# Performance work log

Hardware: AMD Instinct MI355X
Metric: run time of the kernel (lower is better)

Reference implementation:

```python
import jax, jax.numpy as jnp
import numpy as np

B, S, H, D = 2, 4096, 16, 128
TILE = 128
T = S // TILE          # 32 tiles
TOPK = 7               # anchor-selected tiles per query tile (local tile appended -> 8)
DM = H * D
NEG = -1e10


def setup_inputs() -> dict:
    key = jax.random.key(0)
    ks = jax.random.split(key, 6)
    x = jax.random.normal(ks[0], (B, S, DM), dtype=jnp.float32)
    wq = jax.random.normal(ks[1], (DM, H * D), dtype=jnp.float32) * 0.02
    wk = jax.random.normal(ks[2], (DM, H * D), dtype=jnp.float32) * 0.02
    wv = jax.random.normal(ks[3], (DM, H * D), dtype=jnp.float32) * 0.02
    wo = jax.random.normal(ks[4], (H * D, DM), dtype=jnp.float32) * 0.02
    # RoPE tables (real/imag of freqs_cis), LLaMA-style
    inv_freq = 1.0 / (10000.0 ** (np.arange(0, D, 2, dtype=np.float32) / D))  # [D/2]
    t = np.arange(S, dtype=np.float32)
    freqs = np.outer(t, inv_freq)  # [S, D/2]
    cos = jnp.asarray(np.cos(freqs), dtype=jnp.float32)
    sin = jnp.asarray(np.sin(freqs), dtype=jnp.float32)
    anchor_indices = jax.random.randint(ks[5], (B, H, T, TOPK), 0, T, dtype=jnp.int32)
    return {"x": x, "wq": wq, "wk": wk, "wv": wv, "wo": wo,
            "cos": cos, "sin": sin, "anchor_indices": anchor_indices}


def _apply_rope(q, k, cos, sin):
    # q,k: [B,H,S,D]; cos,sin: [S,D/2]
    cos_f = jnp.concatenate([cos, cos], axis=-1)[None, None]  # [1,1,S,D]
    sin_f = jnp.concatenate([sin, sin], axis=-1)[None, None]

    def rot_half(x):
        h = x.shape[-1] // 2
        return jnp.concatenate([-x[..., h:], x[..., :h]], axis=-1)

    return q * cos_f + rot_half(q) * sin_f, k * cos_f + rot_half(k) * sin_f


def reference(x, wq, wk, wv, wo, cos, sin, anchor_indices):
    b, s, _ = x.shape
    h = anchor_indices.shape[1]
    t = anchor_indices.shape[2]
    tile = s // t
    d = wq.shape[1] // h

    q = (x @ wq).reshape(b, s, h, d).transpose(0, 2, 1, 3)  # [B,H,S,D]
    k = (x @ wk).reshape(b, s, h, d).transpose(0, 2, 1, 3)
    v = (x @ wv).reshape(b, s, h, d).transpose(0, 2, 1, 3)
    q, k = _apply_rope(q, k, cos, sin)

    # append local tile to anchor-selected tiles -> [B,H,T,K+1]
    local = jnp.broadcast_to(jnp.arange(t, dtype=jnp.int32)[None, None, :, None], (b, h, t, 1))
    tile_sel = jnp.concatenate([anchor_indices, local], axis=-1)
    # token indices of gathered tiles: [B,H,T,(K+1)*tile]
    offs = jnp.arange(tile, dtype=jnp.int32)[None, None, None, None, :]
    tok_idx = (tile_sel[..., None] * tile + offs)
    sparse_len = tile_sel.shape[-1] * tile
    flat_idx = jnp.clip(tok_idx.reshape(b, h, t, sparse_len), 0, s - 1)

    # gather K/V tiles: [B,H,T,L,D]
    gid = flat_idx.reshape(b, h, t * sparse_len)
    k_sp = jnp.take_along_axis(k, gid[..., None], axis=2).reshape(b, h, t, sparse_len, d)
    v_sp = jnp.take_along_axis(v, gid[..., None], axis=2).reshape(b, h, t, sparse_len, d)

    q_t = q.reshape(b, h, t, tile, d)
    logits = jnp.einsum('bhtqd,bhtkd->bhtqk', q_t, k_sp) / jnp.sqrt(jnp.float32(d))

    # causal future-mask within gathered set
    q_pos = jnp.arange(s, dtype=jnp.int32).reshape(t, tile)
    fut = flat_idx[:, :, :, None, :] > q_pos[None, None, :, :, None]  # [B,H,T,tile,L]
    logits = jnp.where(fut, NEG, logits)
    weights = jax.nn.softmax(logits, axis=-1)
    all_masked = jnp.all(fut, axis=-1, keepdims=True)
    weights = jnp.where(all_masked, 0.0, weights)
    weights = jnp.where(jnp.isnan(weights), 0.0, weights)

    out = jnp.einsum('bhtqk,bhtkd->bhtqd', weights, v_sp)
    out = out.reshape(b, h, s, d).transpose(0, 2, 1, 3).reshape(b, s, h * d)
    return out @ wo
```

## Files before the change

### kernel.cpp

```cpp
#include <hip/hip_runtime.h>
#include <hip/hip_bf16.h>


typedef __bf16 bf16_t;
using bf16x8 = __attribute__((ext_vector_type(8))) __bf16;
using bf16x4 = __attribute__((ext_vector_type(4))) __bf16;
using f32x4  = __attribute__((ext_vector_type(4))) float;

typedef const __attribute__((address_space(1))) void* gas_ptr;
typedef __attribute__((address_space(3))) void* las_ptr;

__device__ __forceinline__ void async_copy16(const void* g, void* l) {
  __builtin_amdgcn_global_load_lds((gas_ptr)g, (las_ptr)l, 16, 0, 0);
}

__device__ __forceinline__ f32x4 mfma16x16x32(bf16x8 a, bf16x8 b, f32x4 c) {
  return __builtin_amdgcn_mfma_f32_16x16x32_bf16(a, b, c, 0, 0, 0);
}

__global__ void prep_kernel(const float* __restrict__ x, const float* __restrict__ wq,
                            const float* __restrict__ wk, const float* __restrict__ wv,
                            const float* __restrict__ wo, bf16_t* __restrict__ xb,
                            bf16_t* __restrict__ wcat, bf16_t* __restrict__ wot) {
  __shared__ bf16_t t[64][66];
  const int bidx = blockIdx.x;
  if (bidx >= 4096) {
    int idx = (bidx - 4096) * 256 + threadIdx.x;
    float4 v = ((const float4*)x)[idx];
    bf16x4 r;
    r.x = (bf16_t)v.x; r.y = (bf16_t)v.y; r.z = (bf16_t)v.z; r.w = (bf16_t)v.w;
    ((bf16x4*)xb)[idx] = r;
    return;
  }
  const int z = bidx >> 10, bt = bidx & 1023;
  const float* W = (z == 0) ? wq : (z == 1) ? wk : (z == 2) ? wv : wo;
  bf16_t* Wt = (z == 3) ? wot : (wcat + (size_t)z * 2048 * 2048);
  const int r0 = (bt >> 5) * 64, c0 = (bt & 31) * 64;
  const int tx = threadIdx.x & 63, ty = threadIdx.x >> 6;
  #pragma unroll
  for (int i = 0; i < 16; ++i) {
    int r = ty + 4 * i;
    t[r][tx] = (bf16_t)W[(size_t)(r0 + r) * 2048 + c0 + tx];
  }
  __syncthreads();
  #pragma unroll
  for (int i = 0; i < 16; ++i) {
    int n = ty + 4 * i;
    Wt[(size_t)(c0 + n) * 2048 + r0 + tx] = t[tx][n];
  }
}

__global__ __launch_bounds__(512, 2) void gemm256(
    const bf16_t* __restrict__ A, const bf16_t* __restrict__ Bt,
    int nb, int mode, float* __restrict__ Cf,
    bf16_t* __restrict__ outQ, bf16_t* __restrict__ outK,
    bf16_t* __restrict__ outVT,
    const float* __restrict__ cosT, const float* __restrict__ sinT)
{
  __shared__ bf16_t Apan[2][16384];
  __shared__ bf16_t Bpan[2][16384];
  const int bid = blockIdx.x;
  const int cpx = gridDim.x >> 3;
  const int swz = (bid & 7) * cpx + (bid >> 3);
  const int RM = cpx / nb;
  const int bm = ((swz / cpx) * RM + (swz % RM)) * 256;
  const int bn = ((swz % cpx) / RM) * 256;
  const int tid = threadIdx.x;
  const int w = tid >> 6, l = tid & 63;
  const int wr = w >> 1, wc = w & 1;
  const int fr = l & 15, g4 = l >> 4;

  const bf16_t* aS[4];
  const bf16_t* bS[4];
  int dst[4];
  #pragma unroll
  for (int i = 0; i < 4; ++i) {
    int c = tid + i * 512;
    int row = c >> 3, ch = c & 7;
    int sc = (ch ^ (row & 7)) * 8;
    aS[i] = A  + (size_t)(bm + row) * 2048 + sc;
    bS[i] = Bt + (size_t)(bn + row) * 2048 + sc;
    dst[i] = c * 16;
  }

  int aOff[2][4], bOff[2][8];
  #pragma unroll
  for (int kc = 0; kc < 2; ++kc) {
    #pragma unroll
    for (int m = 0; m < 4; ++m) {
      int R = wr * 64 + m * 16 + fr;
      aOff[kc][m] = R * 128 + (((kc * 4 + g4) ^ (R & 7)) << 4);
    }
    #pragma unroll
    for (int n = 0; n < 8; ++n) {
      int R = wc * 128 + n * 16 + fr;
      bOff[kc][n] = R * 128 + (((kc * 4 + g4) ^ (R & 7)) << 4);
    }
  }

  f32x4 acc[4][8];
  #pragma unroll
  for (int m = 0; m < 4; ++m)
    #pragma unroll
    for (int n = 0; n < 8; ++n) acc[m][n] = (f32x4){0.f, 0.f, 0.f, 0.f};

  auto STAGE = [&](int t) {
    const int slot = t & 1;
    const int kb = t * 64;
    char* dA = (char*)&Apan[slot][0];
    char* dB = (char*)&Bpan[slot][0];
    #pragma unroll
    for (int i = 0; i < 4; ++i) {
      async_copy16(aS[i] + kb, dA + dst[i]);
      async_copy16(bS[i] + kb, dB + dst[i]);
    }
  };

  STAGE(0);
  __syncthreads();

  #pragma unroll 1
  for (int phi = 0; phi < 32; ++phi) {
    const int slot = phi & 1;
    const char* pa = (const char*)&Apan[slot][0];
    const char* pb = (const char*)&Bpan[slot][0];

    bf16x8 af0[4], bf0[8];
    #pragma unroll
    for (int m = 0; m < 4; ++m) af0[m] = *(const bf16x8*)(pa + aOff[0][m]);
    #pragma unroll
    for (int n = 0; n < 8; ++n) bf0[n] = *(const bf16x8*)(pb + bOff[0][n]);
    if (phi < 31) STAGE(phi + 1);
    __builtin_amdgcn_s_setprio(1);
    #pragma unroll
    for (int m = 0; m < 4; ++m)
      #pragma unroll
      for (int n = 0; n < 8; ++n)
        acc[m][n] = mfma16x16x32(af0[m], bf0[n], acc[m][n]);
    __builtin_amdgcn_s_setprio(0);

    bf16x8 af1[4], bf1[8];
    #pragma unroll
    for (int m = 0; m < 4; ++m) af1[m] = *(const bf16x8*)(pa + aOff[1][m]);
    #pragma unroll
    for (int n = 0; n < 8; ++n) bf1[n] = *(const bf16x8*)(pb + bOff[1][n]);
    __builtin_amdgcn_s_setprio(1);
    #pragma unroll
    for (int m = 0; m < 4; ++m)
      #pragma unroll
      for (int n = 0; n < 8; ++n)
        acc[m][n] = mfma16x16x32(af1[m], bf1[n], acc[m][n]);
    __builtin_amdgcn_s_setprio(0);

    asm volatile("s_waitcnt vmcnt(0)" ::: "memory");
    __builtin_amdgcn_sched_barrier(0);
    __builtin_amdgcn_s_barrier();
    __builtin_amdgcn_sched_barrier(0);
  }

  if (mode == 0) {
    float* S = (w < 4) ? (float*)((char*)&Apan[0][0] + w * 16384)
                       : (float*)((char*)&Bpan[0][0] + (w - 4) * 16384);
    #pragma unroll
    for (int h = 0; h < 2; ++h) {
      #pragma unroll
      for (int mm = 0; mm < 2; ++mm) {
        int m = h * 2 + mm;
        #pragma unroll
        for (int n = 0; n < 8; ++n)
          #pragma unroll
          for (int j = 0; j < 4; ++j)
            S[(mm * 16 + g4 * 4 + j) * 128 + n * 16 + fr] = acc[m][n][j];
      }
      #pragma unroll
      for (int r2 = 0; r2 < 32; ++r2) {
        float2 v = *(const float2*)&S[r2 * 128 + l * 2];
        int row = bm + wr * 64 + h * 32 + r2;
        *(float2*)&Cf[(size_t)row * 2048 + bn + wc * 128 + l * 2] = v;
      }
    }
    return;
  }

  const int colbase = bn + wc * 128;
  const int proj = colbase >> 11;
  const int hh = (colbase & 2047) >> 7;
  if (proj == 2) {
    #pragma unroll
    for (int m = 0; m < 4; ++m) {
      int row0 = bm + wr * 64 + m * 16 + g4 * 4;
      int b_ = row0 >> 12, sr = row0 & 4095;
      #pragma unroll
      for (int n = 0; n < 8; ++n) {
        int d_ = n * 16 + fr;
        bf16x4 pkv;
        #pragma unroll
        for (int j = 0; j < 4; ++j) pkv[j] = (bf16_t)acc[m][n][j];
        *(bf16x4*)&outVT[(((size_t)(b_ * 16 + hh)) * 128 + d_) * 4096 + sr] = pkv;
      }
    }
  } else {
    bf16_t* dst_ = proj ? outK : outQ;
    #pragma unroll
    for (int m = 0; m < 4; ++m) {
      int row0 = bm + wr * 64 + m * 16 + g4 * 4;
      int b_ = row0 >> 12, s0 = row0 & 4095;
      size_t hbase = ((size_t)(b_ * 16 + hh)) * 4096;
      #pragma unroll
      for (int n = 0; n < 4; ++n) {
        int d = n * 16 + fr;
        #pragma unroll
        for (int j = 0; j < 4; ++j) {
          int s = s0 + j;
          float c  = cosT[s * 64 + d];
          float sn = sinT[s * 64 + d];
          float x0 = acc[m][n][j], x1 = acc[m][n + 4][j];
          dst_[(hbase + s) * 128 + d]      = (bf16_t)(x0 * c - x1 * sn);
          dst_[(hbase + s) * 128 + d + 64] = (bf16_t)(x1 * c + x0 * sn);
        }
      }
    }
  }
}

__global__ __launch_bounds__(512, 4) void attn_kernel(
    const bf16_t* __restrict__ Qf, const bf16_t* __restrict__ Kf,
    const bf16_t* __restrict__ Vt, const int* __restrict__ anchors,
    bf16_t* __restrict__ outB)
{
  __shared__ bf16_t Kl[2][8192];
  __shared__ bf16_t Vl[2][8192];
  __shared__ bf16_t Pbuf[8][1024];
  const int orig = blockIdx.x;
  const int blk = (orig & 7) * 128 + (orig >> 3);
  const int qt = 31 - (blk & 31);
  const int h = (blk >> 5) & 15, b = blk >> 9;
  const int bh = b * 16 + h;
  const int tid = threadIdx.x, w = tid >> 6, l = tid & 63;
  const int fr = l & 15, g4 = l >> 4;
  const float scale = 0.08838834764831845f;

  const int* anc = anchors + ((size_t)bh * 32 + qt) * 7;
  unsigned long long pk = 0;
  int nt = 0;
  #pragma unroll
  for (int t = 0; t < 7; ++t) {
    int v = anc[t];
    if (v <= qt) { pk |= (unsigned long long)v << (5 * nt); ++nt; }
  }
  pk |= (unsigned long long)qt << (5 * nt); ++nt;
  const int NS = nt * 2;

  const bf16_t* Qbase = Qf + (size_t)bh * 4096 * 128;
  const bf16_t* Kbase = Kf + (size_t)bh * 4096 * 128;
  const bf16_t* Vbase = Vt + (size_t)bh * 128 * 4096;
  char* P = (char*)&Pbuf[w][0];

  auto STAGE = [&](int tb2, int p) {
    const bf16_t* ksrc = Kbase + (size_t)tb2 * 128;
    const bf16_t* vsrc = Vbase + tb2;
    char* kd = (char*)&Kl[p][0];
    char* vd = (char*)&Vl[p][0];
    #pragma unroll
    for (int i = 0; i < 2; ++i) {
      int c = tid + i * 512;
      int kr = c >> 4, kcol = c & 15;
      async_copy16(ksrc + (size_t)kr * 128 + (size_t)((kcol ^ (kr & 7)) * 8),
                   kd + c * 16);
      int vr = c >> 3, vcol = c & 7;
      async_copy16(vsrc + (size_t)vr * 4096 + (size_t)((vcol ^ (vr & 7)) * 8),
                   vd + c * 16);
    }
  };

  const int qrow = qt * 128 + w * 16 + fr;
  bf16x8 aq[4];
  #pragma unroll
  for (int kc = 0; kc < 4; ++kc)
    aq[kc] = *(const bf16x8*)(Qbase + (size_t)qrow * 128 + kc * 32 + g4 * 8);

  STAGE((int)(pk & 31) * 128, 0);
  __syncthreads();

  float mrun = -1e30f, lrun = 0.f;
  f32x4 o[8];
  #pragma unroll
  for (int nd = 0; nd < 8; ++nd) o[nd] = (f32x4){0.f, 0.f, 0.f, 0.f};

  for (int s = 0; s < NS; ++s) {
    const int p = s & 1;
    const int ts = (int)((pk >> (5 * (s >> 1))) & 31);
    const bool domask = (ts == qt);
    if (s + 1 < NS) {
      int s1 = s + 1;
      int ts1 = (int)((pk >> (5 * (s1 >> 1))) & 31);
      STAGE(ts1 * 128 + (s1 & 1) * 64, p ^ 1);
    }

    f32x4 sc[4];
    #pragma unroll
    for (int n = 0; n < 4; ++n) sc[n] = (f32x4){0.f, 0.f, 0.f, 0.f};
    #pragma unroll
    for (int kc = 0; kc < 4; ++kc) {
      bf16x8 kf[4];
      #pragma unroll
      for (int n = 0; n < 4; ++n) {
        int r = n * 16 + fr;
        kf[n] = *(const bf16x8*)((const char*)&Kl[p][0] +
                 r * 256 + (((kc * 4 + g4) ^ (r & 7)) << 4));
      }
      #pragma unroll
      for (int n = 0; n < 4; ++n)
        sc[n] = mfma16x16x32(kf[n], aq[kc], sc[n]);
    }

    float rmax = -1e30f;
    if (domask) {
      const int qr = w * 16 + fr;
      #pragma unroll
      for (int n = 0; n < 4; ++n)
        #pragma unroll
        for (int j = 0; j < 4; ++j) {
          float lg = sc[n][j] * scale;
          int tok = (s & 1) * 64 + n * 16 + g4 * 4 + j;
          if (tok > qr) lg = -1e10f;
          sc[n][j] = lg;
          rmax = fmaxf(rmax, lg);
        }
    } else {
      #pragma unroll
      for (int n = 0; n < 4; ++n)
        #pragma unroll
        for (int j = 0; j < 4; ++j) {
          float lg = sc[n][j] * scale;
          sc[n][j] = lg;
          rmax = fmaxf(rmax, lg);
        }
    }
    rmax = fmaxf(rmax, __shfl_xor(rmax, 16));
    rmax = fmaxf(rmax, __shfl_xor(rmax, 32));
    if (__any(rmax > mrun + 8.f)) {
      float mnew = fmaxf(mrun, rmax);
      float alpha = __expf(mrun - mnew);
      lrun *= alpha;
      #pragma unroll
      for (int nd = 0; nd < 8; ++nd)
        #pragma unroll
        for (int j = 0; j < 4; ++j) o[nd][j] *= alpha;
      mrun = mnew;
    }
    float rsum = 0.f;
    #pragma unroll
    for (int n = 0; n < 4; ++n) {
      bf16x4 pkv;
      #pragma unroll
      for (int j = 0; j < 4; ++j) {
        float pe = __expf(sc[n][j] - mrun);
        rsum += pe;
        pkv[j] = (bf16_t)pe;
      }
      int off = fr * 128 + ((((n << 1) | (g4 >> 1)) ^ (fr & 7)) << 4) + ((g4 & 1) << 3);
      *(bf16x4*)(P + off) = pkv;
    }
    rsum += __shfl_xor(rsum, 16);
    rsum += __shfl_xor(rsum, 32);
    lrun += rsum;

    #pragma unroll
    for (int kc2 = 0; kc2 < 2; ++kc2) {
      bf16x8 av[8];
      #pragma unroll
      for (int nd = 0; nd < 8; ++nd) {
        int r = nd * 16 + fr;
        av[nd] = *(const bf16x8*)((const char*)&Vl[p][0] +
                  r * 128 + (((kc2 * 4 + g4) ^ (r & 7)) << 4));
      }
      bf16x8 bp = *(const bf16x8*)(P + fr * 128 + ((((kc2 << 2) | g4) ^ (fr & 7)) << 4));
      #pragma unroll
      for (int nd = 0; nd < 8; ++nd)
        o[nd] = mfma16x16x32(av[nd], bp, o[nd]);
    }
    __syncthreads();
  }

  {
    char* E = (char*)&Kl[0][0] + w * 4096;
    float inv = 1.0f / lrun;
    #pragma unroll
    for (int nd = 0; nd < 8; ++nd) {
      bf16x4 pkv;
      #pragma unroll
      for (int j = 0; j < 4; ++j) pkv[j] = (bf16_t)(o[nd][j] * inv);
      int off = fr * 256 + ((((nd << 1) | (g4 >> 1)) ^ (fr & 7)) << 4) + ((g4 & 1) << 3);
      *(bf16x4*)(E + off) = pkv;
    }
    #pragma unroll
    for (int i = 0; i < 4; ++i) {
      int r = i * 4 + g4;
      int off = r * 256 + ((fr ^ (r & 7)) << 4);
      bf16x8 vrow = *(const bf16x8*)(E + off);
      size_t gaddr = (((size_t)b * 4096 + qt * 128 + w * 16 + r) * 2048)
                     + h * 128 + fr * 8;
      *(bf16x8*)(outB + gaddr) = vrow;
    }
  }
}

#define OFF_XB   ((size_t)0)
#define OFF_WCAT ((size_t)33554432)
#define OFF_WOT  ((size_t)58720256)
#define OFF_QF   ((size_t)67108864)
#define OFF_KF   ((size_t)100663296)
#define OFF_AT   ((size_t)134217728)
#define OFF_VT   ((size_t)167772160)

extern "C" void kernel_launch(void* const* d_in, const int* in_sizes, int n_in,
                              void* d_out, int out_size, void* d_ws, size_t ws_size,
                              hipStream_t stream) {
  (void)in_sizes; (void)n_in; (void)out_size; (void)ws_size;
  const float* x    = (const float*)d_in[0];
  const float* wq   = (const float*)d_in[1];
  const float* wk   = (const float*)d_in[2];
  const float* wv   = (const float*)d_in[3];
  const float* wo   = (const float*)d_in[4];
  const float* cosT = (const float*)d_in[5];
  const float* sinT = (const float*)d_in[6];
  const int*   anc  = (const int*)d_in[7];
  float* out = (float*)d_out;
  char* ws = (char*)d_ws;

  bf16_t* xb   = (bf16_t*)(ws + OFF_XB);
  bf16_t* wcat = (bf16_t*)(ws + OFF_WCAT);
  bf16_t* wot  = (bf16_t*)(ws + OFF_WOT);
  bf16_t* Qf   = (bf16_t*)(ws + OFF_QF);
  bf16_t* Kf   = (bf16_t*)(ws + OFF_KF);
  bf16_t* Vt   = (bf16_t*)(ws + OFF_VT);
  bf16_t* attnB = (bf16_t*)(ws + OFF_AT);

  prep_kernel<<<20480, 256, 0, stream>>>(x, wq, wk, wv, wo, xb, wcat, wot);
  gemm256<<<768, 512, 0, stream>>>(xb, wcat, 24, 1, nullptr, Qf, Kf, Vt, cosT, sinT);
  attn_kernel<<<1024, 512, 0, stream>>>(Qf, Kf, Vt, anc, attnB);
  gemm256<<<256, 512, 0, stream>>>(attnB, wot, 8, 0, out, nullptr, nullptr, nullptr,
                                   nullptr, nullptr);
}
```

Measured before the change: 351.9 us.

## Single-buffer K/V in attention with staggered loads to cut LDS footprint

Replaces the double-buffered K and V shared-memory tiles with single buffers. The next K chunk is issued after the QK^T phase and the next V chunk after the PV phase, with explicit vmcnt waits and raw barriers. This shrinks LDS per block so more attention blocks can reside per CU. In exchange it adds extra barriers per step and exposes more load latency, since each prefetch overlaps only part of one iteration.

```diff
diff --git a/kernel.cpp b/kernel.cpp
--- a/kernel.cpp
+++ b/kernel.cpp
@@ -17,6 +17,8 @@
 __device__ __forceinline__ f32x4 mfma16x16x32(bf16x8 a, bf16x8 b, f32x4 c) {
   return __builtin_amdgcn_mfma_f32_16x16x32_bf16(a, b, c, 0, 0, 0);
 }
+
+#define SBAR0() __builtin_amdgcn_sched_barrier(0)
 
 __global__ void prep_kernel(const float* __restrict__ x, const float* __restrict__ wq,
                             const float* __restrict__ wk, const float* __restrict__ wv,
@@ -153,9 +155,9 @@
     __builtin_amdgcn_s_setprio(0);
 
     asm volatile("s_waitcnt vmcnt(0)" ::: "memory");
-    __builtin_amdgcn_sched_barrier(0);
+    SBAR0();
     __builtin_amdgcn_s_barrier();
-    __builtin_amdgcn_sched_barrier(0);
+    SBAR0();
   }
 
   if (mode == 0) {
@@ -228,9 +230,10 @@
     const bf16_t* __restrict__ Vt, const int* __restrict__ anchors,
     bf16_t* __restrict__ outB)
 {
-  __shared__ bf16_t Kl[2][8192];
-  __shared__ bf16_t Vl[2][8192];
-  __shared__ bf16_t Pbuf[8][1024];
+  __shared__ bf16_t SH[24576];
+  bf16_t* Kl = SH;
+  bf16_t* Vl = SH + 8192;
+  bf16_t* Pb = SH + 16384;
   const int orig = blockIdx.x;
   const int blk = (orig & 7) * 128 + (orig >> 3);
   const int qt = 31 - (blk & 31);
@@ -254,22 +257,26 @@
   const bf16_t* Qbase = Qf + (size_t)bh * 4096 * 128;
   const bf16_t* Kbase = Kf + (size_t)bh * 4096 * 128;
   const bf16_t* Vbase = Vt + (size_t)bh * 128 * 4096;
-  char* P = (char*)&Pbuf[w][0];
-
-  auto STAGE = [&](int tb2, int p) {
+  char* P = (char*)(Pb + w * 1024);
+
+  auto STAGE_K = [&](int tb2) {
     const bf16_t* ksrc = Kbase + (size_t)tb2 * 128;
-    const bf16_t* vsrc = Vbase + tb2;
-    char* kd = (char*)&Kl[p][0];
-    char* vd = (char*)&Vl[p][0];
     #pragma unroll
     for (int i = 0; i < 2; ++i) {
       int c = tid + i * 512;
       int kr = c >> 4, kcol = c & 15;
       async_copy16(ksrc + (size_t)kr * 128 + (size_t)((kcol ^ (kr & 7)) * 8),
-                   kd + c * 16);
+                   (char*)Kl + c * 16);
+    }
+  };
+  auto STAGE_V = [&](int tb2) {
+    const bf16_t* vsrc = Vbase + tb2;
+    #pragma unroll
+    for (int i = 0; i < 2; ++i) {
+      int c = tid + i * 512;
       int vr = c >> 3, vcol = c & 7;
       async_copy16(vsrc + (size_t)vr * 4096 + (size_t)((vcol ^ (vr & 7)) * 8),
-                   vd + c * 16);
+                   (char*)Vl + c * 16);
     }
   };
 
@@ -279,8 +286,13 @@
   for (int kc = 0; kc < 4; ++kc)
     aq[kc] = *(const bf16x8*)(Qbase + (size_t)qrow * 128 + kc * 32 + g4 * 8);
 
-  STAGE((int)(pk & 31) * 128, 0);
-  __syncthreads();
+  {
+    int tb0 = (int)(pk & 31) * 128;
+    STAGE_K(tb0);
+    STAGE_V(tb0);
+    asm volatile("s_waitcnt vmcnt(2)" ::: "memory");
+    SBAR0(); __builtin_amdgcn_s_barrier(); SBAR0();
+  }
 
   float mrun = -1e30f, lrun = 0.f;
   f32x4 o[8];
@@ -288,13 +300,13 @@
   for (int nd = 0; nd < 8; ++nd) o[nd] = (f32x4){0.f, 0.f, 0.f, 0.f};
 
   for (int s = 0; s < NS; ++s) {
-    const int p = s & 1;
     const int ts = (int)((pk >> (5 * (s >> 1))) & 31);
     const bool domask = (ts == qt);
-    if (s + 1 < NS) {
+    const bool more = (s + 1 < NS);
+    int ntb = 0;
+    if (more) {
       int s1 = s + 1;
-      int ts1 = (int)((pk >> (5 * (s1 >> 1))) & 31);
-      STAGE(ts1 * 128 + (s1 & 1) * 64, p ^ 1);
+      ntb = (int)((pk >> (5 * (s1 >> 1))) & 31) * 128 + (s1 & 1) * 64;
     }
 
     f32x4 sc[4];
@@ -306,13 +318,17 @@
       #pragma unroll
       for (int n = 0; n < 4; ++n) {
         int r = n * 16 + fr;
-        kf[n] = *(const bf16x8*)((const char*)&Kl[p][0] +
+        kf[n] = *(const bf16x8*)((const char*)Kl +
                  r * 256 + (((kc * 4 + g4) ^ (r & 7)) << 4));
       }
       #pragma unroll
       for (int n = 0; n < 4; ++n)
         sc[n] = mfma16x16x32(kf[n], aq[kc], sc[n]);
     }
+
+    asm volatile("s_waitcnt vmcnt(0)" ::: "memory");
+    SBAR0(); __builtin_amdgcn_s_barrier(); SBAR0();
+    if (more) STAGE_K(ntb);
 
     float rmax = -1e30f;
     if (domask) {
@@ -372,7 +388,7 @@
       #pragma unroll
       for (int nd = 0; nd < 8; ++nd) {
         int r = nd * 16 + fr;
-        av[nd] = *(const bf16x8*)((const char*)&Vl[p][0] +
+        av[nd] = *(const bf16x8*)((const char*)Vl +
                   r * 128 + (((kc2 * 4 + g4) ^ (r & 7)) << 4));
       }
       bf16x8 bp = *(const bf16x8*)(P + fr * 128 + ((((kc2 << 2) | g4) ^ (fr & 7)) << 4));
@@ -380,11 +396,17 @@
       for (int nd = 0; nd < 8; ++nd)
         o[nd] = mfma16x16x32(av[nd], bp, o[nd]);
     }
-    __syncthreads();
+
+    SBAR0(); __builtin_amdgcn_s_barrier(); SBAR0();
+    if (more) {
+      STAGE_V(ntb);
+      asm volatile("s_waitcnt vmcnt(2)" ::: "memory");
+      SBAR0(); __builtin_amdgcn_s_barrier(); SBAR0();
+    }
   }
 
   {
-    char* E = (char*)&Kl[0][0] + w * 4096;
+    char* E = (char*)SH + w * 4096;
     float inv = 1.0f / lrun;
     #pragma unroll
     for (int nd = 0; nd < 8; ++nd) {
```

After: 352.2 us (median of 2 runs). No clear change (+0.1%).
